# Performance work log

Measured on AMD Instinct MI355X. Metric: run time of the kernel, lower is better.

## Reference

```python
import jax, jax.numpy as jnp
import numpy as np

MODES = 4
WIDTH = 8
IN_CH = 3
OUT_CH = 6
LAMBDA_RES = 0.3


def spectral_conv3d(x, w1, w2, w3, w4):
    # x: [B, C, D, H, W] real. Standard FNO3d SpectralConv3d:
    # rfftn over last 3 dims, multiply low modes in 4 corner octants, irfftn.
    B, C, D, H, W = x.shape
    m = MODES
    x_ft = jnp.fft.rfftn(x, axes=(-3, -2, -1))  # [B,C,D,H,W//2+1] complex

    def mul(blk, w):
        return jnp.einsum('bixyz,ioxyz->boxyz', blk, w)

    out_ft = jnp.zeros((B, w1.shape[1], D, H, W // 2 + 1), dtype=x_ft.dtype)
    out_ft = out_ft.at[:, :, :m, :m, :m].set(mul(x_ft[:, :, :m, :m, :m], w1))
    out_ft = out_ft.at[:, :, -m:, :m, :m].set(mul(x_ft[:, :, -m:, :m, :m], w2))
    out_ft = out_ft.at[:, :, :m, -m:, :m].set(mul(x_ft[:, :, :m, -m:, :m], w3))
    out_ft = out_ft.at[:, :, -m:, -m:, :m].set(mul(x_ft[:, :, -m:, -m:, :m], w4))
    return jnp.fft.irfftn(out_ft, s=(D, H, W), axes=(-3, -2, -1))


def fno3d(u, fc0_w, fc0_b, spec_ws, conv_ws, conv_bs, fc1_w, fc1_b, fc2_w, fc2_b):
    # Lift: 1x1 conv via einsum (channels-first)
    x = jnp.einsum('bcdhw,oc->bodhw', u, fc0_w) + fc0_b[None, :, None, None, None]
    for i in range(4):
        w1, w2, w3, w4 = spec_ws[i]
        x1 = spectral_conv3d(x, w1, w2, w3, w4)
        x2 = jnp.einsum('bcdhw,oc->bodhw', x, conv_ws[i]) + conv_bs[i][None, :, None, None, None]
        x = x1 + x2
        if i < 3:
            x = jax.nn.gelu(x)
    x = jnp.einsum('bcdhw,oc->bodhw', x, fc1_w) + fc1_b[None, :, None, None, None]
    x = jax.nn.gelu(x)
    x = jnp.einsum('bcdhw,oc->bodhw', x, fc2_w) + fc2_b[None, :, None, None, None]
    return x


def setup_inputs() -> dict:
    key = jax.random.key(0)
    ks = jax.random.split(key, 32)
    B, D, H, W = 8, 64, 64, 64
    m, wd = MODES, WIDTH
    u = jax.random.normal(ks[0], (B, IN_CH, D, H, W), dtype=jnp.float32)
    scale = 1.0 / (wd * wd)
    spec_ws = []
    ki = 1
    for _ in range(4):
        layer = []
        for _ in range(4):
            re = jax.random.uniform(ks[ki], (wd, wd, m, m, m)) * scale
            im = jax.random.uniform(ks[ki + 1], (wd, wd, m, m, m)) * scale
            layer.append(re + 1j * im)
            ki += 2
        spec_ws.append(tuple(layer))
    conv_ws = [jax.random.normal(ks[ki + i], (wd, wd)) * (1.0 / wd) for i in range(4)]
    ki += 4
    conv_bs = [jnp.zeros((wd,), jnp.float32) for _ in range(4)]
    fc0_w = jax.random.normal(ks[ki], (wd, IN_CH)) * 0.3; ki += 1
    fc0_b = jnp.zeros((wd,), jnp.float32)
    fc1_w = jax.random.normal(ks[ki], (4 * wd, wd)) * 0.2; ki += 1
    fc1_b = jnp.zeros((4 * wd,), jnp.float32)
    fc2_w = jax.random.normal(ks[ki], (OUT_CH, 4 * wd)) * 0.2; ki += 1
    fc2_b = jnp.zeros((OUT_CH,), jnp.float32)
    nu = jnp.asarray(0.001, jnp.float32)
    return {
        'u': u, 'nu': nu,
        'fc0_w': fc0_w, 'fc0_b': fc0_b,
        'spec_ws': spec_ws, 'conv_ws': conv_ws, 'conv_bs': conv_bs,
        'fc1_w': fc1_w, 'fc1_b': fc1_b, 'fc2_w': fc2_w, 'fc2_b': fc2_b,
    }


def reference(u, nu, fc0_w, fc0_b, spec_ws, conv_ws, conv_bs, fc1_w, fc1_b, fc2_w, fc2_b):
    B, C, D, H, W = u.shape
    # hard core: zeros [B,6,D,H,W] with first 3 channels = u*nu
    hard = jnp.concatenate([u * nu, jnp.zeros((B, 3, D, H, W), u.dtype)], axis=1)
    soft = fno3d(u, fc0_w, fc0_b, spec_ws, conv_ws, conv_bs, fc1_w, fc1_b, fc2_w, fc2_b)
    return hard + LAMBDA_RES * soft
```

## Files before the change

kernel.cpp:

```cpp
#include <hip/hip_runtime.h>


#define TWO_PI_OVER_64 0.09817477042468103

typedef float v2f __attribute__((ext_vector_type(2)));

__device__ __forceinline__ float gelu_fast(float x) {
    float x2 = x * x;
    float p  = x * (1.0f + 0.044715f * x2);
    float e  = __builtin_amdgcn_exp2f(-2.3022083f * p);
    return x * __builtin_amdgcn_rcpf(1.0f + e);
}

__device__ __forceinline__ v2f gelu2(v2f x) {
    v2f x2 = x * x;
    v2f p  = x * (1.0f + 0.044715f * x2);
    v2f r;
    r.x = __builtin_amdgcn_rcpf(1.0f + __builtin_amdgcn_exp2f(-2.3022083f * p.x));
    r.y = __builtin_amdgcn_rcpf(1.0f + __builtin_amdgcn_exp2f(-2.3022083f * p.y));
    return x * r;
}

#define BUILD_TW() \
    __shared__ float twc[64], tws[64]; \
    if (threadIdx.x < 64) { \
        double a_ = TWO_PI_OVER_64 * (double)threadIdx.x; \
        twc[threadIdx.x] = (float)cos(a_); tws[threadIdx.x] = (float)sin(a_); \
    }

#define LOAD_WTW() \
    v2f c1p[2], s1p[2], c2p[2], s2p[2], c3p[2], s3p[2]; \
    _Pragma("unroll") \
    for (int p = 0; p < 2; ++p) { \
        int wa = wq * 4 + 2 * p, wb = wa + 1; \
        c1p[p] = (v2f){twc[wa], twc[wb]}; \
        s1p[p] = (v2f){tws[wa], tws[wb]}; \
        c2p[p] = (v2f){twc[(2 * wa) & 63], twc[(2 * wb) & 63]}; \
        s2p[p] = (v2f){tws[(2 * wa) & 63], tws[(2 * wb) & 63]}; \
        c3p[p] = (v2f){twc[(3 * wa) & 63], twc[(3 * wb) & 63]}; \
        s3p[p] = (v2f){tws[(3 * wa) & 63], tws[(3 * wb) & 63]}; \
    }

#define ROR_STEP(x, CTRL) \
    x += __int_as_float(__builtin_amdgcn_update_dpp( \
            0, __float_as_int(x), CTRL, 0xF, 0xF, true))

__device__ __forceinline__ float red16_ror(float x) {
    ROR_STEP(x, 0x121);
    ROR_STEP(x, 0x122);
    ROR_STEP(x, 0x124);
    ROR_STEP(x, 0x128);
    return x;
}

__device__ __forceinline__ float addswap1(float x) {
    return x + __int_as_float(__builtin_amdgcn_update_dpp(
            0, __float_as_int(x), 0xB1, 0xF, 0xF, true));
}

__device__ __forceinline__ void a_tail_store(
    const v2f v[2], const v2f c1[2], const v2f s1[2],
    const v2f c2[2], const v2f s2[2], const v2f c3[2], const v2f s3[2],
    int wq, float2* __restrict__ Arow)
{
    v2f d;
    d = v[0] + v[1];               float p0  = d.x + d.y;
    d = v[0]*c1[0] + v[1]*c1[1];   float ar1 = d.x + d.y;
    d = v[0]*s1[0] + v[1]*s1[1];   float ai1 = -(d.x + d.y);
    d = v[0]*c2[0] + v[1]*c2[1];   float ar2 = d.x + d.y;
    d = v[0]*s2[0] + v[1]*s2[1];   float ai2 = -(d.x + d.y);
    d = v[0]*c3[0] + v[1]*c3[1];   float ar3 = d.x + d.y;
    d = v[0]*s3[0] + v[1]*s3[1];   float ai3 = -(d.x + d.y);
    p0  = red16_ror(p0);
    ar1 = red16_ror(ar1);  ai1 = red16_ror(ai1);
    ar2 = red16_ror(ar2);  ai2 = red16_ror(ai2);
    ar3 = red16_ror(ar3);  ai3 = red16_ror(ai3);
    if (wq < 2) {
        float4 av;
        av.x = (wq == 0) ? p0   : ar2;
        av.y = (wq == 0) ? 0.f  : ai2;
        av.z = (wq == 0) ? ar1  : ar3;
        av.w = (wq == 0) ? ai1  : ai3;
        *((float4*)Arow + wq) = av;
    }
}

__global__ __launch_bounds__(256) void k_liftA(
    const float* __restrict__ u, const float* __restrict__ fc0w,
    const float* __restrict__ fc0b, float* __restrict__ x,
    float2* __restrict__ A)
{
    BUILD_TW();
    const int t = threadIdx.x, bid = blockIdx.x;
    const int b = bid >> 8, dx = (bid >> 2) & 63, dy0 = (bid & 3) * 16;
    const int dyl = t >> 4, wq = t & 15;
    const size_t sp = (size_t)dx * 4096 + (size_t)(dy0 + dyl) * 64 + wq * 4;
    v2f uin[3][2];
    #pragma unroll
    for (int c = 0; c < 3; ++c) {
        float4 v = *(const float4*)&u[(size_t)(b * 3 + c) * 262144 + sp];
        uin[c][0] = (v2f){v.x, v.y};
        uin[c][1] = (v2f){v.z, v.w};
    }
    __syncthreads();
    LOAD_WTW();
    #pragma unroll
    for (int o = 0; o < 8; ++o) {
        float w0 = fc0w[o * 3 + 0], w1 = fc0w[o * 3 + 1], w2 = fc0w[o * 3 + 2];
        float bb = fc0b[o];
        v2f vp[2];
        #pragma unroll
        for (int p = 0; p < 2; ++p)
            vp[p] = bb + uin[0][p] * w0 + uin[1][p] * w1 + uin[2][p] * w2;
        *(float4*)&x[(size_t)(b * 8 + o) * 262144 + sp] =
            make_float4(vp[0].x, vp[0].y, vp[1].x, vp[1].y);
        a_tail_store(vp, c1p, s1p, c2p, s2p, c3p, s3p, wq,
                     A + ((size_t)(b * 8 + o) * 4096 + dx * 64 + dy0 + dyl) * 4);
    }
}

__global__ __launch_bounds__(256) void k_fH(const float2* __restrict__ A,
                                            float2* __restrict__ Bh)
{
    BUILD_TW();
    __syncthreads();
    const int g = blockIdx.x * 256 + threadIdx.x;
    const int pid = g >> 1, half = g & 1;
    const int kz2 = (pid & 1) * 2;
    const int ky  = (pid >> 1) & 7;
    const int dx  = (pid >> 4) & 63;
    const int c   = (pid >> 10) & 7;
    const int b   = pid >> 13;
    const int kyv = ky < 4 ? ky : ky + 56;
    const float2* Ap = A + (size_t)(b * 8 + c) * 16384 + dx * 256 + half * 4 + kz2;
    float re0 = 0.f, im0 = 0.f, re1 = 0.f, im1 = 0.f;
    int ti = (kyv * half) & 63;
    const int step = (kyv * 2) & 63;
    #pragma unroll 8
    for (int i = 0; i < 32; ++i) {
        float4 a = *(const float4*)&Ap[i * 8];
        float cc = twc[ti], ss = tws[ti];
        re0 += a.x * cc + a.y * ss;
        im0 += a.y * cc - a.x * ss;
        re1 += a.z * cc + a.w * ss;
        im1 += a.w * cc - a.z * ss;
        ti = (ti + step) & 63;
    }
    re0 = addswap1(re0);  im0 = addswap1(im0);
    re1 = addswap1(re1);  im1 = addswap1(im1);
    if (half == 0)
        *(float4*)&Bh[(size_t)(b * 8 + c) * 2048 + dx * 32 + ky * 4 + kz2] =
            make_float4(re0, im0, re1, im1);
}

__global__ __launch_bounds__(256) void k_fDmix(
    const float2* __restrict__ Bh,
    const float2* __restrict__ w1, const float2* __restrict__ w2,
    const float2* __restrict__ w3, const float2* __restrict__ w4,
    float2* __restrict__ O)
{
    BUILD_TW();
    __shared__ float2 Cs[256];
    const int t = threadIdx.x, bid = blockIdx.x;
    const int b = bid >> 3, kx = bid & 7;
    const int kxv = kx < 4 ? kx : kx + 56;
    __syncthreads();
    {
        int kz = t & 3, ky = (t >> 2) & 7, c = t >> 5;
        const float2* Bp = Bh + (size_t)(b * 8 + c) * 2048 + ky * 4 + kz;
        float re = 0.f, im = 0.f;
        int ti = 0;
        #pragma unroll 8
        for (int dx = 0; dx < 64; ++dx) {
            float2 v = Bp[dx * 32];
            float cc = twc[ti], ss = tws[ti];
            re += v.x * cc + v.y * ss;
            im += v.y * cc - v.x * ss;
            ti = (ti + kxv) & 63;
        }
        Cs[t] = make_float2(re, im);
    }
    __syncthreads();
    {
        int kz = t & 3, ky = (t >> 2) & 7, o = t >> 5;
        const float2* wsel = (kx < 4) ? ((ky < 4) ? w1 : w3) : ((ky < 4) ? w2 : w4);
        int kxw = kx & 3, kyw = ky & 3;
        float re = 0.f, im = 0.f;
        #pragma unroll
        for (int i = 0; i < 8; ++i) {
            float2 cv = Cs[i * 32 + ky * 4 + kz];
            float2 wv = wsel[(((size_t)(i * 8 + o) * 4 + kxw) * 4 + kyw) * 4 + kz];
            re += cv.x * wv.x - cv.y * wv.y;
            im += cv.x * wv.y + cv.y * wv.x;
        }
        O[(((size_t)(b * 8 + o) * 8 + kx) * 8 + ky) * 4 + kz] = make_float2(re, im);
    }
}

__global__ __launch_bounds__(256, 4) void k_ptA(
    float* __restrict__ x, const float2* __restrict__ O,
    const float* __restrict__ cw, const float* __restrict__ cb,
    float2* __restrict__ A)
{
    BUILD_TW();
    __shared__ float2 Ps[256];
    __shared__ float2 Qs[8 * 16 * 4];
    const int t = threadIdx.x, bid = blockIdx.x;
    const int b = bid >> 8, dx = (bid >> 2) & 63, dy0 = (bid & 3) * 16;
    const int dyl = t >> 4, wq = t & 15;
    const size_t sp = (size_t)dx * 4096 + (size_t)(dy0 + dyl) * 64 + wq * 4;
    float4 xv[8];
    #pragma unroll
    for (int c = 0; c < 8; ++c)
        xv[c] = *(const float4*)&x[(size_t)(b * 8 + c) * 262144 + sp];
    const int pkz = t & 3, pky = (t >> 2) & 7, po = t >> 5;
    float2 ov[8];
    #pragma unroll
    for (int kxi = 0; kxi < 8; ++kxi)
        ov[kxi] = O[(((size_t)(b * 8 + po) * 8 + kxi) * 8 + pky) * 4 + pkz];
    __syncthreads();
    {
        float re = 0.f, im = 0.f;
        #pragma unroll
        for (int kxi = 0; kxi < 8; ++kxi) {
            int kxv = kxi < 4 ? kxi : kxi + 56;
            int ti = (kxv * dx) & 63;
            float cc = twc[ti], ss = tws[ti];
            re += ov[kxi].x * cc - ov[kxi].y * ss;
            im += ov[kxi].y * cc + ov[kxi].x * ss;
        }
        Ps[t] = make_float2(re, im);
    }
    __syncthreads();
    for (int it = t; it < 512; it += 256) {
        int kz = it & 3, qdyl = (it >> 2) & 15, o = it >> 6;
        int dy = dy0 + qdyl;
        float re = 0.f, im = 0.f;
        #pragma unroll
        for (int kyi = 0; kyi < 8; ++kyi) {
            int kyv = kyi < 4 ? kyi : kyi + 56;
            int ti = (kyv * dy) & 63;
            float2 v = Ps[(o * 8 + kyi) * 4 + kz];
            float cc = twc[ti], ss = tws[ti];
            re += v.x * cc - v.y * ss;
            im += v.y * cc + v.x * ss;
        }
        Qs[(o * 16 + qdyl) * 4 + kz] = make_float2(re, im);
    }
    __syncthreads();
    LOAD_WTW();
    const float invN3 = 1.0f / 262144.0f;
    #pragma unroll
    for (int o = 0; o < 8; ++o) {
        float4 qa = *(const float4*)&Qs[(o * 16 + dyl) * 4];
        float4 qb = *(const float4*)&Qs[(o * 16 + dyl) * 4 + 2];
        const float cbo = cb[o];
        v2f outp[2];
        #pragma unroll
        for (int p = 0; p < 2; ++p) {
            v2f x1 = qa.x + 2.f * (qa.z * c1p[p] - qa.w * s1p[p]
                                 + qb.x * c2p[p] - qb.y * s2p[p]
                                 + qb.z * c3p[p] - qb.w * s3p[p]);
            x1 *= invN3;
            v2f x2 = (v2f){cbo, cbo};
            #pragma unroll
            for (int c = 0; c < 8; ++c) {
                const v2f* xp = (const v2f*)&xv[c];
                x2 += cw[o * 8 + c] * xp[p];
            }
            outp[p] = gelu2(x1 + x2);
        }
        *(float4*)&x[(size_t)(b * 8 + o) * 262144 + sp] =
            make_float4(outp[0].x, outp[0].y, outp[1].x, outp[1].y);
        a_tail_store(outp, c1p, s1p, c2p, s2p, c3p, s3p, wq,
                     A + ((size_t)(b * 8 + o) * 4096 + dx * 64 + dy0 + dyl) * 4);
    }
}

__global__ __launch_bounds__(256, 4) void k_ptout(
    const float* __restrict__ x, const float2* __restrict__ O,
    const float* __restrict__ cw, const float* __restrict__ cb,
    const float* __restrict__ u, const float* __restrict__ nu,
    const float* __restrict__ fc1w, const float* __restrict__ fc1b,
    const float* __restrict__ fc2w, const float* __restrict__ fc2b,
    float* __restrict__ out)
{
    BUILD_TW();
    __shared__ float2 Ps[256];
    __shared__ float2 Qs[8 * 16 * 4];
    const int t = threadIdx.x, bid = blockIdx.x;
    const int b = bid >> 8, dx = (bid >> 2) & 63, dy0 = (bid & 3) * 16;
    const int dyl = t >> 4, wq = t & 15;
    const size_t sp = (size_t)dx * 4096 + (size_t)(dy0 + dyl) * 64 + wq * 4;
    float4 xv[8];
    #pragma unroll
    for (int c = 0; c < 8; ++c)
        xv[c] = *(const float4*)&x[(size_t)(b * 8 + c) * 262144 + sp];
    float4 uv[3];
    #pragma unroll
    for (int c = 0; c < 3; ++c)
        uv[c] = *(const float4*)&u[(size_t)(b * 3 + c) * 262144 + sp];
    const int pkz = t & 3, pky = (t >> 2) & 7, po = t >> 5;
    float2 ovv[8];
    #pragma unroll
    for (int kxi = 0; kxi < 8; ++kxi)
        ovv[kxi] = O[(((size_t)(b * 8 + po) * 8 + kxi) * 8 + pky) * 4 + pkz];
    __syncthreads();
    {
        float re = 0.f, im = 0.f;
        #pragma unroll
        for (int kxi = 0; kxi < 8; ++kxi) {
            int kxv = kxi < 4 ? kxi : kxi + 56;
            int ti = (kxv * dx) & 63;
            float cc = twc[ti], ss = tws[ti];
            re += ovv[kxi].x * cc - ovv[kxi].y * ss;
            im += ovv[kxi].y * cc + ovv[kxi].x * ss;
        }
        Ps[t] = make_float2(re, im);
    }
    __syncthreads();
    for (int it = t; it < 512; it += 256) {
        int kz = it & 3, qdyl = (it >> 2) & 15, o = it >> 6;
        int dy = dy0 + qdyl;
        float re = 0.f, im = 0.f;
        #pragma unroll
        for (int kyi = 0; kyi < 8; ++kyi) {
            int kyv = kyi < 4 ? kyi : kyi + 56;
            int ti = (kyv * dy) & 63;
            float2 v = Ps[(o * 8 + kyi) * 4 + kz];
            float cc = twc[ti], ss = tws[ti];
            re += v.x * cc - v.y * ss;
            im += v.y * cc + v.x * ss;
        }
        Qs[(o * 16 + qdyl) * 4 + kz] = make_float2(re, im);
    }
    __syncthreads();
    LOAD_WTW();
    const float invN3 = 1.0f / 262144.0f;
    v2f vvp[8][2];
    #pragma unroll
    for (int o = 0; o < 8; ++o) {
        float4 qa = *(const float4*)&Qs[(o * 16 + dyl) * 4];
        float4 qb = *(const float4*)&Qs[(o * 16 + dyl) * 4 + 2];
        const float cbo = cb[o];
        #pragma unroll
        for (int p = 0; p < 2; ++p) {
            v2f x1 = qa.x + 2.f * (qa.z * c1p[p] - qa.w * s1p[p]
                                 + qb.x * c2p[p] - qb.y * s2p[p]
                                 + qb.z * c3p[p] - qb.w * s3p[p]);
            x1 *= invN3;
            v2f x2 = (v2f){cbo, cbo};
            #pragma unroll
            for (int c = 0; c < 8; ++c) {
                const v2f* xp = (const v2f*)&xv[c];
                x2 += cw[o * 8 + c] * xp[p];
            }
            vvp[o][p] = x1 + x2;
        }
    }
    v2f so2[6][2];
    #pragma unroll
    for (int c6 = 0; c6 < 6; ++c6) {
        float bb = fc2b[c6];
        so2[c6][0] = (v2f){bb, bb};
        so2[c6][1] = (v2f){bb, bb};
    }
    #pragma unroll 8
    for (int h = 0; h < 32; ++h) {
        float wr[8];
        #pragma unroll
        for (int c = 0; c < 8; ++c) wr[c] = fc1w[h * 8 + c];
        const float hb = fc1b[h];
        float w2r[6];
        #pragma unroll
        for (int c6 = 0; c6 < 6; ++c6) w2r[c6] = fc2w[c6 * 32 + h];
        #pragma unroll
        for (int p = 0; p < 2; ++p) {
            v2f a = (v2f){hb, hb};
            #pragma unroll
            for (int c = 0; c < 8; ++c) a += vvp[c][p] * wr[c];
            v2f g = gelu2(a);
            #pragma unroll
            for (int c6 = 0; c6 < 6; ++c6) so2[c6][p] += g * w2r[c6];
        }
    }
    const float nuv = nu[0];
    #pragma unroll
    for (int c6 = 0; c6 < 6; ++c6) {
        v2f r0 = 0.3f * so2[c6][0];
        v2f r1 = 0.3f * so2[c6][1];
        if (c6 < 3) {
            const v2f* up = (const v2f*)&uv[c6];
            r0 += up[0] * nuv;
            r1 += up[1] * nuv;
        }
        *(float4*)&out[(size_t)(b * 6 + c6) * 262144 + sp] =
            make_float4(r0.x, r0.y, r1.x, r1.y);
    }
}

struct PackPtrs { const float* re[16]; const float* im[16]; };

__global__ __launch_bounds__(256) void k_pack_all(PackPtrs p, float2* __restrict__ dst)
{
    int i = blockIdx.x * 256 + threadIdx.x;
    int w = i >> 12, idx = i & 4095;
    dst[i] = make_float2(p.re[w][idx], p.im[w][idx]);
}

extern "C" void kernel_launch(void* const* d_in, const int* in_sizes, int n_in,
                              void* d_out, int out_size, void* d_ws, size_t ws_size,
                              hipStream_t stream)
{
    (void)out_size;
    const char* leaf[32];
    bool spec_split = false;
    const char* spec_re[16]; const char* spec_im[16];
    int src = 0;
    leaf[0] = (const char*)d_in[src++];
    leaf[1] = (const char*)d_in[src++];
    leaf[2] = (const char*)d_in[src++];
    leaf[3] = (const char*)d_in[src++];
    {
        int s = (src < n_in) ? in_sizes[src] : 4096;
        if (n_in >= 48 && s == 4096) {
            spec_split = true;
            for (int i = 0; i < 16; ++i) {
                spec_re[i] = (const char*)d_in[src++];
                spec_im[i] = (const char*)d_in[src++];
            }
        } else {
            int per;
            if (s == 4096 || s == 8192) per = 1;
            else if (s == 16384 || s == 32768) per = 4;
            else per = 16;
            for (int i = 0; i < 16; i += per) {
                const char* base = (const char*)d_in[src++];
                for (int j = 0; j < per; ++j) leaf[4 + i + j] = base + (size_t)j * 4096 * 8;
            }
        }
    }
    {
        int s = (src < n_in) ? in_sizes[src] : 64;
        if (s == 64) { for (int i = 0; i < 4; ++i) leaf[20 + i] = (const char*)d_in[src++]; }
        else { const char* base = (const char*)d_in[src++];
               for (int i = 0; i < 4; ++i) leaf[20 + i] = base + (size_t)i * 64 * 4; }
    }
    {
        int s = (src < n_in) ? in_sizes[src] : 8;
        if (s == 8) { for (int i = 0; i < 4; ++i) leaf[24 + i] = (const char*)d_in[src++]; }
        else { const char* base = (const char*)d_in[src++];
               for (int i = 0; i < 4; ++i) leaf[24 + i] = base + (size_t)i * 8 * 4; }
    }
    leaf[28] = (const char*)d_in[src++];
    leaf[29] = (const char*)d_in[src++];
    leaf[30] = (const char*)d_in[src++];
    leaf[31] = (const char*)d_in[src++];

    const float* u    = (const float*)leaf[0];
    const float* nu   = (const float*)leaf[1];
    const float* fc0w = (const float*)leaf[2];
    const float* fc0b = (const float*)leaf[3];
    const float* convw[4], *convb[4];
    for (int i = 0; i < 4; ++i) { convw[i] = (const float*)leaf[20 + i];
                                  convb[i] = (const float*)leaf[24 + i]; }
    const float* fc1w = (const float*)leaf[28];
    const float* fc1b = (const float*)leaf[29];
    const float* fc2w = (const float*)leaf[30];
    const float* fc2b = (const float*)leaf[31];

    const size_t szX = 67108864, szA = 8388608, szB = 1048576,
                 szO = 131072, szSP = 524288;
    char* ws = (char*)d_ws;
    float* xbuf = (float*)ws;
    float2 *Abuf, *Bbuf, *Obuf, *SP;
    if (ws_size >= szX + szA + szB + szO + szSP) {
        Abuf = (float2*)(ws + szX);
        Bbuf = (float2*)(ws + szX + szA);
        Obuf = (float2*)(ws + szX + szA + szB);
        SP   = (float2*)(ws + szX + szA + szB + szO);
    } else {
        Obuf = (float2*)(ws + szX);
        Abuf = (float2*)d_out;
        Bbuf = (float2*)((char*)d_out + szA);
        SP   = (float2*)((char*)d_out + szA + szB);
    }

    const float2* specw[16];
    if (spec_split) {
        PackPtrs pp;
        for (int i = 0; i < 16; ++i) {
            pp.re[i] = (const float*)spec_re[i];
            pp.im[i] = (const float*)spec_im[i];
            specw[i] = SP + (size_t)i * 4096;
        }
        hipLaunchKernelGGL(k_pack_all, dim3(256), dim3(256), 0, stream, pp, SP);
    } else {
        for (int i = 0; i < 16; ++i) specw[i] = (const float2*)leaf[4 + i];
    }
    float* outp = (float*)d_out;

    hipLaunchKernelGGL(k_liftA, dim3(2048), dim3(256), 0, stream, u, fc0w, fc0b, xbuf, Abuf);
    for (int L = 0; L < 4; ++L) {
        hipLaunchKernelGGL(k_fH, dim3(512), dim3(256), 0, stream, Abuf, Bbuf);
        hipLaunchKernelGGL(k_fDmix, dim3(64), dim3(256), 0, stream,
                           Bbuf, specw[L*4+0], specw[L*4+1], specw[L*4+2], specw[L*4+3], Obuf);
        if (L < 3) {
            hipLaunchKernelGGL(k_ptA, dim3(2048), dim3(256), 0, stream,
                               xbuf, Obuf, convw[L], convb[L], Abuf);
        } else {
            hipLaunchKernelGGL(k_ptout, dim3(2048), dim3(256), 0, stream,
                               xbuf, Obuf, convw[3], convb[3], u, nu,
                               fc1w, fc1b, fc2w, fc2b, outp);
        }
    }
}
```

Before: 279.8 us.

## Process two dy tiles per block in pointwise kernels to reuse Ps and twiddles

The k_ptA and k_ptout kernels now each handle two 16-row dy tiles per block, halving the grid from 2048 to 1024 blocks. Twiddle setup, the O loads and the kx-stage Ps computation are done once and shared by both tiles. The second tile's x and u loads are issued after the first tile's Q stage so they overlap with compute. In exchange each block does twice the work, adds LDS and register pressure, and the grid has fewer blocks to spread across the GPU.

```diff
diff --git a/kernel.cpp b/kernel.cpp
--- a/kernel.cpp
+++ b/kernel.cpp
@@ -4,13 +4,6 @@
 #define TWO_PI_OVER_64 0.09817477042468103
 
 typedef float v2f __attribute__((ext_vector_type(2)));
-
-__device__ __forceinline__ float gelu_fast(float x) {
-    float x2 = x * x;
-    float p  = x * (1.0f + 0.044715f * x2);
-    float e  = __builtin_amdgcn_exp2f(-2.3022083f * p);
-    return x * __builtin_amdgcn_rcpf(1.0f + e);
-}
 
 __device__ __forceinline__ v2f gelu2(v2f x) {
     v2f x2 = x * x;
@@ -204,15 +197,19 @@
 {
     BUILD_TW();
     __shared__ float2 Ps[256];
-    __shared__ float2 Qs[8 * 16 * 4];
+    __shared__ float2 QsA[8 * 16 * 4];
+    __shared__ float2 QsB[8 * 16 * 4];
     const int t = threadIdx.x, bid = blockIdx.x;
-    const int b = bid >> 8, dx = (bid >> 2) & 63, dy0 = (bid & 3) * 16;
+    const int b = bid >> 7, rem = bid & 127;
+    const int dx = rem >> 1, dyh = rem & 1;
     const int dyl = t >> 4, wq = t & 15;
-    const size_t sp = (size_t)dx * 4096 + (size_t)(dy0 + dyl) * 64 + wq * 4;
-    float4 xv[8];
+    const int dy0_0 = dyh * 32, dy0_1 = dyh * 32 + 16;
+    const size_t sp0 = (size_t)dx * 4096 + (size_t)(dy0_0 + dyl) * 64 + wq * 4;
+    const size_t sp1 = (size_t)dx * 4096 + (size_t)(dy0_1 + dyl) * 64 + wq * 4;
+    float4 xv1[8];
     #pragma unroll
     for (int c = 0; c < 8; ++c)
-        xv[c] = *(const float4*)&x[(size_t)(b * 8 + c) * 262144 + sp];
+        xv1[c] = *(const float4*)&x[(size_t)(b * 8 + c) * 262144 + sp0];
     const int pkz = t & 3, pky = (t >> 2) & 7, po = t >> 5;
     float2 ov[8];
     #pragma unroll
@@ -234,7 +231,7 @@
     __syncthreads();
     for (int it = t; it < 512; it += 256) {
         int kz = it & 3, qdyl = (it >> 2) & 15, o = it >> 6;
-        int dy = dy0 + qdyl;
+        int dy = dy0_0 + qdyl;
         float re = 0.f, im = 0.f;
         #pragma unroll
         for (int kyi = 0; kyi < 8; ++kyi) {
@@ -245,15 +242,19 @@
             re += v.x * cc - v.y * ss;
             im += v.y * cc + v.x * ss;
         }
-        Qs[(o * 16 + qdyl) * 4 + kz] = make_float2(re, im);
-    }
-    __syncthreads();
+        QsA[(o * 16 + qdyl) * 4 + kz] = make_float2(re, im);
+    }
+    __syncthreads();
+    float4 xv2[8];
+    #pragma unroll
+    for (int c = 0; c < 8; ++c)
+        xv2[c] = *(const float4*)&x[(size_t)(b * 8 + c) * 262144 + sp1];
     LOAD_WTW();
     const float invN3 = 1.0f / 262144.0f;
     #pragma unroll
     for (int o = 0; o < 8; ++o) {
-        float4 qa = *(const float4*)&Qs[(o * 16 + dyl) * 4];
-        float4 qb = *(const float4*)&Qs[(o * 16 + dyl) * 4 + 2];
+        float4 qa = *(const float4*)&QsA[(o * 16 + dyl) * 4];
+        float4 qb = *(const float4*)&QsA[(o * 16 + dyl) * 4 + 2];
         const float cbo = cb[o];
         v2f outp[2];
         #pragma unroll
@@ -265,15 +266,56 @@
             v2f x2 = (v2f){cbo, cbo};
             #pragma unroll
             for (int c = 0; c < 8; ++c) {
-                const v2f* xp = (const v2f*)&xv[c];
+                const v2f* xp = (const v2f*)&xv1[c];
                 x2 += cw[o * 8 + c] * xp[p];
             }
             outp[p] = gelu2(x1 + x2);
         }
-        *(float4*)&x[(size_t)(b * 8 + o) * 262144 + sp] =
+        *(float4*)&x[(size_t)(b * 8 + o) * 262144 + sp0] =
             make_float4(outp[0].x, outp[0].y, outp[1].x, outp[1].y);
         a_tail_store(outp, c1p, s1p, c2p, s2p, c3p, s3p, wq,
-                     A + ((size_t)(b * 8 + o) * 4096 + dx * 64 + dy0 + dyl) * 4);
+                     A + ((size_t)(b * 8 + o) * 4096 + dx * 64 + dy0_0 + dyl) * 4);
+    }
+    for (int it = t; it < 512; it += 256) {
+        int kz = it & 3, qdyl = (it >> 2) & 15, o = it >> 6;
+        int dy = dy0_1 + qdyl;
+        float re = 0.f, im = 0.f;
+        #pragma unroll
+        for (int kyi = 0; kyi < 8; ++kyi) {
+            int kyv = kyi < 4 ? kyi : kyi + 56;
+            int ti = (kyv * dy) & 63;
+            float2 v = Ps[(o * 8 + kyi) * 4 + kz];
+            float cc = twc[ti], ss = tws[ti];
+            re += v.x * cc - v.y * ss;
+            im += v.y * cc + v.x * ss;
+        }
+        QsB[(o * 16 + qdyl) * 4 + kz] = make_float2(re, im);
+    }
+    __syncthreads();
+    #pragma unroll
+    for (int o = 0; o < 8; ++o) {
+        float4 qa = *(const float4*)&QsB[(o * 16 + dyl) * 4];
+        float4 qb = *(const float4*)&QsB[(o * 16 + dyl) * 4 + 2];
+        const float cbo = cb[o];
+        v2f outp[2];
+        #pragma unroll
+        for (int p = 0; p < 2; ++p) {
+            v2f x1 = qa.x + 2.f * (qa.z * c1p[p] - qa.w * s1p[p]
+                                 + qb.x * c2p[p] - qb.y * s2p[p]
+                                 + qb.z * c3p[p] - qb.w * s3p[p]);
+            x1 *= invN3;
+            v2f x2 = (v2f){cbo, cbo};
+            #pragma unroll
+            for (int c = 0; c < 8; ++c) {
+                const v2f* xp = (const v2f*)&xv2[c];
+                x2 += cw[o * 8 + c] * xp[p];
+            }
+            outp[p] = gelu2(x1 + x2);
+        }
+        *(float4*)&x[(size_t)(b * 8 + o) * 262144 + sp1] =
+            make_float4(outp[0].x, outp[0].y, outp[1].x, outp[1].y);
+        a_tail_store(outp, c1p, s1p, c2p, s2p, c3p, s3p, wq,
+                     A + ((size_t)(b * 8 + o) * 4096 + dx * 64 + dy0_1 + dyl) * 4);
     }
 }
 
@@ -287,19 +329,24 @@
 {
     BUILD_TW();
     __shared__ float2 Ps[256];
-    __shared__ float2 Qs[8 * 16 * 4];
+    __shared__ float2 QsA[8 * 16 * 4];
+    __shared__ float2 QsB[8 * 16 * 4];
     const int t = threadIdx.x, bid = blockIdx.x;
-    const int b = bid >> 8, dx = (bid >> 2) & 63, dy0 = (bid & 3) * 16;
+    const int b = bid >> 7, rem = bid & 127;
+    const int dx = rem >> 1, dyh = rem & 1;
     const int dyl = t >> 4, wq = t & 15;
-    const size_t sp = (size_t)dx * 4096 + (size_t)(dy0 + dyl) * 64 + wq * 4;
-    float4 xv[8];
+    const int dy0_0 = dyh * 32, dy0_1 = dyh * 32 + 16;
+    const size_t sp0 = (size_t)dx * 4096 + (size_t)(dy0_0 + dyl) * 64 + wq * 4;
+    const size_t sp1 = (size_t)dx * 4096 + (size_t)(dy0_1 + dyl) * 64 + wq * 4;
+    const float invN3 = 1.0f / 262144.0f;
+    float4 xv1[8];
     #pragma unroll
     for (int c = 0; c < 8; ++c)
-        xv[c] = *(const float4*)&x[(size_t)(b * 8 + c) * 262144 + sp];
-    float4 uv[3];
+        xv1[c] = *(const float4*)&x[(size_t)(b * 8 + c) * 262144 + sp0];
+    float4 uv1[3];
     #pragma unroll
     for (int c = 0; c < 3; ++c)
-        uv[c] = *(const float4*)&u[(size_t)(b * 3 + c) * 262144 + sp];
+        uv1[c] = *(const float4*)&u[(size_t)(b * 3 + c) * 262144 + sp0];
     const int pkz = t & 3, pky = (t >> 2) & 7, po = t >> 5;
     float2 ovv[8];
     #pragma unroll
@@ -321,7 +368,7 @@
     __syncthreads();
     for (int it = t; it < 512; it += 256) {
         int kz = it & 3, qdyl = (it >> 2) & 15, o = it >> 6;
-        int dy = dy0 + qdyl;
+        int dy = dy0_0 + qdyl;
         float re = 0.f, im = 0.f;
         #pragma unroll
         for (int kyi = 0; kyi < 8; ++kyi) {
@@ -332,16 +379,16 @@
             re += v.x * cc - v.y * ss;
             im += v.y * cc + v.x * ss;
         }
-        Qs[(o * 16 + qdyl) * 4 + kz] = make_float2(re, im);
+        QsA[(o * 16 + qdyl) * 4 + kz] = make_float2(re, im);
     }
     __syncthreads();
     LOAD_WTW();
-    const float invN3 = 1.0f / 262144.0f;
+    const float nuv = nu[0];
     v2f vvp[8][2];
     #pragma unroll
     for (int o = 0; o < 8; ++o) {
-        float4 qa = *(const float4*)&Qs[(o * 16 + dyl) * 4];
-        float4 qb = *(const float4*)&Qs[(o * 16 + dyl) * 4 + 2];
+        float4 qa = *(const float4*)&QsA[(o * 16 + dyl) * 4];
+        float4 qb = *(const float4*)&QsA[(o * 16 + dyl) * 4 + 2];
         const float cbo = cb[o];
         #pragma unroll
         for (int p = 0; p < 2; ++p) {
@@ -352,50 +399,135 @@
             v2f x2 = (v2f){cbo, cbo};
             #pragma unroll
             for (int c = 0; c < 8; ++c) {
-                const v2f* xp = (const v2f*)&xv[c];
+                const v2f* xp = (const v2f*)&xv1[c];
                 x2 += cw[o * 8 + c] * xp[p];
             }
             vvp[o][p] = x1 + x2;
         }
     }
-    v2f so2[6][2];
-    #pragma unroll
-    for (int c6 = 0; c6 < 6; ++c6) {
-        float bb = fc2b[c6];
-        so2[c6][0] = (v2f){bb, bb};
-        so2[c6][1] = (v2f){bb, bb};
-    }
-    #pragma unroll 8
-    for (int h = 0; h < 32; ++h) {
-        float wr[8];
-        #pragma unroll
-        for (int c = 0; c < 8; ++c) wr[c] = fc1w[h * 8 + c];
-        const float hb = fc1b[h];
-        float w2r[6];
-        #pragma unroll
-        for (int c6 = 0; c6 < 6; ++c6) w2r[c6] = fc2w[c6 * 32 + h];
+    float4 xv2[8];
+    #pragma unroll
+    for (int c = 0; c < 8; ++c)
+        xv2[c] = *(const float4*)&x[(size_t)(b * 8 + c) * 262144 + sp1];
+    {
+        v2f so2[6][2];
+        #pragma unroll
+        for (int c6 = 0; c6 < 6; ++c6) {
+            float bb = fc2b[c6];
+            so2[c6][0] = (v2f){bb, bb};
+            so2[c6][1] = (v2f){bb, bb};
+        }
+        #pragma unroll 8
+        for (int h = 0; h < 32; ++h) {
+            float wr[8];
+            #pragma unroll
+            for (int c = 0; c < 8; ++c) wr[c] = fc1w[h * 8 + c];
+            const float hb = fc1b[h];
+            float w2r[6];
+            #pragma unroll
+            for (int c6 = 0; c6 < 6; ++c6) w2r[c6] = fc2w[c6 * 32 + h];
+            #pragma unroll
+            for (int p = 0; p < 2; ++p) {
+                v2f a = (v2f){hb, hb};
+                #pragma unroll
+                for (int c = 0; c < 8; ++c) a += vvp[c][p] * wr[c];
+                v2f g = gelu2(a);
+                #pragma unroll
+                for (int c6 = 0; c6 < 6; ++c6) so2[c6][p] += g * w2r[c6];
+            }
+        }
+        #pragma unroll
+        for (int c6 = 0; c6 < 6; ++c6) {
+            v2f r0 = 0.3f * so2[c6][0];
+            v2f r1 = 0.3f * so2[c6][1];
+            if (c6 < 3) {
+                const v2f* up = (const v2f*)&uv1[c6];
+                r0 += up[0] * nuv;
+                r1 += up[1] * nuv;
+            }
+            *(float4*)&out[(size_t)(b * 6 + c6) * 262144 + sp0] =
+                make_float4(r0.x, r0.y, r1.x, r1.y);
+        }
+    }
+    float4 uv2[3];
+    #pragma unroll
+    for (int c = 0; c < 3; ++c)
+        uv2[c] = *(const float4*)&u[(size_t)(b * 3 + c) * 262144 + sp1];
+    for (int it = t; it < 512; it += 256) {
+        int kz = it & 3, qdyl = (it >> 2) & 15, o = it >> 6;
+        int dy = dy0_1 + qdyl;
+        float re = 0.f, im = 0.f;
+        #pragma unroll
+        for (int kyi = 0; kyi < 8; ++kyi) {
+            int kyv = kyi < 4 ? kyi : kyi + 56;
+            int ti = (kyv * dy) & 63;
+            float2 v = Ps[(o * 8 + kyi) * 4 + kz];
+            float cc = twc[ti], ss = tws[ti];
+            re += v.x * cc - v.y * ss;
+            im += v.y * cc + v.x * ss;
+        }
+        QsB[(o * 16 + qdyl) * 4 + kz] = make_float2(re, im);
+    }
+    __syncthreads();
+    #pragma unroll
+    for (int o = 0; o < 8; ++o) {
+        float4 qa = *(const float4*)&QsB[(o * 16 + dyl) * 4];
+        float4 qb = *(const float4*)&QsB[(o * 16 + dyl) * 4 + 2];
+        const float cbo = cb[o];
         #pragma unroll
         for (int p = 0; p < 2; ++p) {
-            v2f a = (v2f){hb, hb};
-            #pragma unroll
-            for (int c = 0; c < 8; ++c) a += vvp[c][p] * wr[c];
-            v2f g = gelu2(a);
-            #pragma unroll
-            for (int c6 = 0; c6 < 6; ++c6) so2[c6][p] += g * w2r[c6];
-        }
-    }
-    const float nuv = nu[0];
-    #pragma unroll
-    for (int c6 = 0; c6 < 6; ++c6) {
-        v2f r0 = 0.3f * so2[c6][0];
-        v2f r1 = 0.3f * so2[c6][1];
-        if (c6 < 3) {
-            const v2f* up = (const v2f*)&uv[c6];
-            r0 += up[0] * nuv;
-            r1 += up[1] * nuv;
-        }
-        *(float4*)&out[(size_t)(b * 6 + c6) * 262144 + sp] =
-            make_float4(r0.x, r0.y, r1.x, r1.y);
+            v2f x1 = qa.x + 2.f * (qa.z * c1p[p] - qa.w * s1p[p]
+                                 + qb.x * c2p[p] - qb.y * s2p[p]
+                                 + qb.z * c3p[p] - qb.w * s3p[p]);
+            x1 *= invN3;
+            v2f x2 = (v2f){cbo, cbo};
+            #pragma unroll
+            for (int c = 0; c < 8; ++c) {
+                const v2f* xp = (const v2f*)&xv2[c];
+                x2 += cw[o * 8 + c] * xp[p];
+            }
+            vvp[o][p] = x1 + x2;
+        }
+    }
+    {
+        v2f so2[6][2];
+        #pragma unroll
+        for (int c6 = 0; c6 < 6; ++c6) {
+            float bb = fc2b[c6];
+            so2[c6][0] = (v2f){bb, bb};
+            so2[c6][1] = (v2f){bb, bb};
+        }
+        #pragma unroll 8
+        for (int h = 0; h < 32; ++h) {
+            float wr[8];
+            #pragma unroll
+            for (int c = 0; c < 8; ++c) wr[c] = fc1w[h * 8 + c];
+            const float hb = fc1b[h];
+            float w2r[6];
+            #pragma unroll
+            for (int c6 = 0; c6 < 6; ++c6) w2r[c6] = fc2w[c6 * 32 + h];
+            #pragma unroll
+            for (int p = 0; p < 2; ++p) {
+                v2f a = (v2f){hb, hb};
+                #pragma unroll
+                for (int c = 0; c < 8; ++c) a += vvp[c][p] * wr[c];
+                v2f g = gelu2(a);
+                #pragma unroll
+                for (int c6 = 0; c6 < 6; ++c6) so2[c6][p] += g * w2r[c6];
+            }
+        }
+        #pragma unroll
+        for (int c6 = 0; c6 < 6; ++c6) {
+            v2f r0 = 0.3f * so2[c6][0];
+            v2f r1 = 0.3f * so2[c6][1];
+            if (c6 < 3) {
+                const v2f* up = (const v2f*)&uv2[c6];
+                r0 += up[0] * nuv;
+                r1 += up[1] * nuv;
+            }
+            *(float4*)&out[(size_t)(b * 6 + c6) * 262144 + sp1] =
+                make_float4(r0.x, r0.y, r1.x, r1.y);
+        }
     }
 }
 
@@ -506,10 +638,10 @@
         hipLaunchKernelGGL(k_fDmix, dim3(64), dim3(256), 0, stream,
                            Bbuf, specw[L*4+0], specw[L*4+1], specw[L*4+2], specw[L*4+3], Obuf);
         if (L < 3) {
-            hipLaunchKernelGGL(k_ptA, dim3(2048), dim3(256), 0, stream,
+            hipLaunchKernelGGL(k_ptA, dim3(1024), dim3(256), 0, stream,
                                xbuf, Obuf, convw[L], convb[L], Abuf);
         } else {
-            hipLaunchKernelGGL(k_ptout, dim3(2048), dim3(256), 0, stream,
+            hipLaunchKernelGGL(k_ptout, dim3(1024), dim3(256), 0, stream,
                                xbuf, Obuf, convw[3], convb[3], u, nu,
                                fc1w, fc1b, fc2w, fc2b, outp);
         }
```

Result: slower. 308.4 us (+10.2%).
